# Optimization experiments

Hardware: AMD Instinct MI355X
Metric: run time of the kernel (lower is better)

Reference implementation:

```python
import jax, jax.numpy as jnp
import numpy as np

N_NODES = 100000
N_EDGES = 50000
NNZ = 1600000
IN_DIM, HID_DIM, N_CLASSES = 128, 128, 16


def setup_inputs() -> dict:
    key = jax.random.key(0)
    k1, k2, k3, k4, k5 = jax.random.split(key, 5)
    x = jax.random.normal(k1, (N_NODES, IN_DIM), dtype=jnp.float32)
    node_idx = jax.random.randint(k2, (NNZ,), 0, N_NODES, dtype=jnp.int64)
    edge_idx = jax.random.randint(k3, (NNZ,), 0, N_EDGES, dtype=jnp.int64)
    # glorot-ish weights, zero bias (PyG HypergraphConv: Linear(bias=False) + bias Parameter)
    W1 = jax.random.normal(k4, (IN_DIM, HID_DIM), dtype=jnp.float32) * (1.0 / np.sqrt(IN_DIM))
    b1 = jnp.zeros((HID_DIM,), dtype=jnp.float32)
    W2 = jax.random.normal(k5, (HID_DIM, N_CLASSES), dtype=jnp.float32) * (1.0 / np.sqrt(HID_DIM))
    b2 = jnp.zeros((N_CLASSES,), dtype=jnp.float32)
    return {"x": x, "node_idx": node_idx, "edge_idx": edge_idx, "num_edges": N_EDGES,
            "W1": W1, "b1": b1, "W2": W2, "b2": b2}


def hypergraph_conv(x, W, b, node_idx, edge_idx, num_edges):
    """PyG HypergraphConv (no attention, unit hyperedge weights):
       out = D^{-1} H B^{-1} H^T (x W) + b
    implemented as gather -> segment_sum (node->edge) -> gather -> segment_sum (edge->node)."""
    n_nodes = x.shape[0]
    ones = jnp.ones(node_idx.shape[0], dtype=x.dtype)
    deg = jax.ops.segment_sum(ones, node_idx, num_segments=n_nodes)      # D: node degree
    edeg = jax.ops.segment_sum(ones, edge_idx, num_segments=num_edges)   # B: hyperedge size
    Dinv = jnp.where(deg > 0, 1.0 / deg, 0.0)
    Binv = jnp.where(edeg > 0, 1.0 / edeg, 0.0)

    xw = x @ W                                                            # [N, F_out]
    # node -> hyperedge, norm = B^{-1} applied per message (indexed by edge)
    msg_ne = xw[node_idx] * Binv[edge_idx][:, None]                       # [nnz, F_out]
    e_feat = jax.ops.segment_sum(msg_ne, edge_idx, num_segments=num_edges)
    # hyperedge -> node, norm = D^{-1} applied per message (indexed by node)
    msg_en = e_feat[edge_idx] * Dinv[node_idx][:, None]                   # [nnz, F_out]
    out = jax.ops.segment_sum(msg_en, node_idx, num_segments=n_nodes)
    return out + b


def reference(x, node_idx, edge_idx, num_edges, W1, b1, W2, b2):
    # Dropout is inactive in eval mode; model is relu(conv1) -> conv2.
    h = jax.nn.relu(hypergraph_conv(x, W1, b1, node_idx, edge_idx, num_edges))
    return hypergraph_conv(h, W2, b2, node_idx, edge_idx, num_edges)
```

## Files before the change

### kernel.cpp

```cpp
#include <hip/hip_runtime.h>
#include <hip/hip_fp16.h>


#define N_EDGES_C 50000
#define F1 128
#define F2 16
#define CHUNK 4096
#define EBIN_SHIFT 7
#define NBIN_SHIFT 8
#define EBINS 391
#define NBINS 391

typedef __attribute__((ext_vector_type(8))) _Float16 half8;
typedef __attribute__((ext_vector_type(4))) float f32x4;
typedef unsigned short ushort16_t;


__global__ __launch_bounds__(256) void hist_chunk_kernel(
    const int* __restrict__ node_idx, const int* __restrict__ edge_idx,
    int* __restrict__ echunkcnt, int* __restrict__ nchunkcnt, int nnz) {
  __shared__ int ebc[EBINS], nbc[NBINS];
  const int t = threadIdx.x;
  for (int b = t; b < EBINS; b += 256) ebc[b] = 0;
  for (int b = t; b < NBINS; b += 256) nbc[b] = 0;
  __syncthreads();
  const int base = blockIdx.x * CHUNK;
  int end = base + CHUNK; if (end > nnz) end = nnz;
  for (int i = base + t; i < end; i += 256) {
    atomicAdd(&ebc[edge_idx[i] >> EBIN_SHIFT], 1);
    atomicAdd(&nbc[node_idx[i] >> NBIN_SHIFT], 1);
  }
  __syncthreads();
  const int nC = gridDim.x;
  for (int b = t; b < EBINS; b += 256) echunkcnt[b * nC + blockIdx.x] = ebc[b];
  for (int b = t; b < NBINS; b += 256) nchunkcnt[b * nC + blockIdx.x] = nbc[b];
}

__global__ __launch_bounds__(256) void cscan_p1_kernel(
    const int* __restrict__ ecc, const int* __restrict__ ncc,
    int* __restrict__ epart, int* __restrict__ npart,
    int Le, int Ln, int nbE) {
  __shared__ int red[256];
  const int t = threadIdx.x;
  const int b = blockIdx.x;
  const int* src; int L; int* dst; int bb;
  if (b < nbE) { src = ecc; L = Le; dst = epart; bb = b; }
  else         { src = ncc; L = Ln; dst = npart; bb = b - nbE; }
  int base = bb * 1024 + t * 4;
  int s = 0;
#pragma unroll
  for (int j = 0; j < 4; ++j) { int i = base + j; if (i < L) s += src[i]; }
  red[t] = s;
  __syncthreads();
  for (int d = 128; d > 0; d >>= 1) {
    if (t < d) red[t] += red[t + d];
    __syncthreads();
  }
  if (t == 0) dst[bb] = red[0];
}

__global__ __launch_bounds__(256) void cscan_p2_kernel(
    int* __restrict__ epart, int* __restrict__ npart,
    int* __restrict__ ebinbase, int* __restrict__ nbinbase,
    int nbE, int nbN, int nnz) {
  __shared__ int se[256], sn[256];
  const int t = threadIdx.x;
  se[t] = (t < nbE) ? epart[t] : 0;
  sn[t] = (t < nbN) ? npart[t] : 0;
  __syncthreads();
  for (int d = 1; d < 256; d <<= 1) {
    int ve = (t >= d) ? se[t - d] : 0;
    int vn = (t >= d) ? sn[t - d] : 0;
    __syncthreads();
    se[t] += ve; sn[t] += vn;
    __syncthreads();
  }
  if (t < nbE) epart[t] = (t > 0) ? se[t - 1] : 0;
  if (t < nbN) npart[t] = (t > 0) ? sn[t - 1] : 0;
  if (t == 0) { ebinbase[EBINS] = nnz; nbinbase[NBINS] = nnz; }
}

__global__ __launch_bounds__(256) void cscan_p3_kernel(
    const int* __restrict__ ecc, const int* __restrict__ ncc,
    const int* __restrict__ epart, const int* __restrict__ npart,
    int* __restrict__ erunoff, int* __restrict__ nrunoff,
    int* __restrict__ ebinbase, int* __restrict__ nbinbase,
    int Le, int Ln, int nbE, int nC) {
  __shared__ int red[256];
  const int t = threadIdx.x;
  const int b = blockIdx.x;
  const int* src; const int* part; int L; int* ro; int* bba; int bb;
  if (b < nbE) { src = ecc; part = epart; L = Le; ro = erunoff; bba = ebinbase; bb = b; }
  else         { src = ncc; part = npart; L = Ln; ro = nrunoff; bba = nbinbase; bb = b - nbE; }
  int base = bb * 1024 + t * 4;
  int v[4]; int s = 0;
#pragma unroll
  for (int j = 0; j < 4; ++j) { int i = base + j; v[j] = (i < L) ? src[i] : 0; s += v[j]; }
  red[t] = s;
  __syncthreads();
  for (int d = 1; d < 256; d <<= 1) {
    int x = (t >= d) ? red[t - d] : 0;
    __syncthreads();
    red[t] += x;
    __syncthreads();
  }
  int run = part[bb] + ((t > 0) ? red[t - 1] : 0);
#pragma unroll
  for (int j = 0; j < 4; ++j) {
    int i = base + j;
    if (i < L) {
      ro[i] = run;
      if (i % nC == 0) bba[i / nC] = run;
      run += v[j];
    }
  }
}


__global__ __launch_bounds__(256) void stage_kernel(
    const int* __restrict__ node_idx, const int* __restrict__ edge_idx,
    const int* __restrict__ erunoff, const int* __restrict__ nrunoff,
    unsigned* __restrict__ epairs, unsigned* __restrict__ npairs, int nnz) {
  __shared__ int ecur[EBINS], ncur[NBINS];
  const int t = threadIdx.x;
  const int nC = gridDim.x;
  for (int b = t; b < EBINS; b += 256) ecur[b] = erunoff[b * nC + blockIdx.x];
  for (int b = t; b < NBINS; b += 256) ncur[b] = nrunoff[b * nC + blockIdx.x];
  __syncthreads();
  const int base = blockIdx.x * CHUNK;
  int end = base + CHUNK; if (end > nnz) end = nnz;
  for (int i = base + t; i < end; i += 256) {
    int e = edge_idx[i];
    int n = node_idx[i];
    int p = atomicAdd(&ecur[e >> EBIN_SHIFT], 1);
    epairs[p] = ((unsigned)n << 7) | (unsigned)(e & 127);
    int q = atomicAdd(&ncur[n >> NBIN_SHIFT], 1);
    npairs[q] = ((unsigned)e << 8) | (unsigned)(n & 255);
  }
}

__global__ __launch_bounds__(256) void bin_scatter_kernel(
    const unsigned* __restrict__ epairs, const unsigned* __restrict__ npairs,
    const int* __restrict__ ebinbase, const int* __restrict__ nbinbase,
    int* __restrict__ eoff, int* __restrict__ noff,
    int* __restrict__ enbr, ushort16_t* __restrict__ nnbr,
    int n_edges, int n_nodes) {
  __shared__ int cnt[256];
  __shared__ int scn[256];
  const int bid = blockIdx.x;
  const int t = threadIdx.x;
  if (bid < EBINS) {
    const int e0 = bid << EBIN_SHIFT;
    const int ne = min(1 << EBIN_SHIFT, n_edges - e0);
    const int beg = ebinbase[bid], end = ebinbase[bid + 1];
    if (t < 128) cnt[t] = 0;
    __syncthreads();
    for (int j = beg + t; j < end; j += 256) atomicAdd(&cnt[epairs[j] & 127u], 1);
    __syncthreads();
    if (t < 128) scn[t] = cnt[t];
    __syncthreads();
    for (int d = 1; d < 128; d <<= 1) {
      int x = 0;
      if (t < 128 && t >= d) x = scn[t - d];
      __syncthreads();
      if (t < 128) scn[t] += x;
      __syncthreads();
    }
    int pos0 = 0;
    if (t < 128) {
      int excl = (t > 0) ? scn[t - 1] : 0;
      pos0 = beg + excl;
      if (t < ne) eoff[e0 + t] = pos0;
    }
    __syncthreads();
    if (t < 128) scn[t] = pos0;
    __syncthreads();
    for (int j = beg + t; j < end; j += 256) {
      unsigned p = epairs[j];
      int pos = atomicAdd(&scn[p & 127u], 1);
      enbr[pos] = (int)(p >> 7);
    }
    if (bid == EBINS - 1 && t == 0) eoff[n_edges] = end;
  } else {
    const int b = bid - EBINS;
    const int n0 = b << NBIN_SHIFT;
    const int nn = min(1 << NBIN_SHIFT, n_nodes - n0);
    const int beg = nbinbase[b], end = nbinbase[b + 1];
    cnt[t] = 0;
    __syncthreads();
    for (int j = beg + t; j < end; j += 256) atomicAdd(&cnt[npairs[j] & 255u], 1);
    __syncthreads();
    scn[t] = cnt[t];
    __syncthreads();
    for (int d = 1; d < 256; d <<= 1) {
      int x = (t >= d) ? scn[t - d] : 0;
      __syncthreads();
      scn[t] += x;
      __syncthreads();
    }
    int excl = (t > 0) ? scn[t - 1] : 0;
    int pos0 = beg + excl;
    if (t < nn) noff[n0 + t] = pos0;
    __syncthreads();
    scn[t] = pos0;
    __syncthreads();
    for (int j = beg + t; j < end; j += 256) {
      unsigned p = npairs[j];
      int pos = atomicAdd(&scn[p & 255u], 1);
      nnbr[pos] = (ushort16_t)(p >> 8);
    }
    if (bid == EBINS + NBINS - 1 && t == 0) noff[n_nodes] = end;
  }
}


__global__ __launch_bounds__(256) void w1t_kernel(
    const float* __restrict__ W1, __half* __restrict__ W1t) {
  int i = blockIdx.x * 256 + threadIdx.x;
  int n = i >> 7, k = i & 127;
  W1t[i] = __float2half(W1[k * 128 + n]);
}


__global__ __launch_bounds__(256) void gemm1_kernel(
    const float* __restrict__ A, const __half* __restrict__ W1t16,
    __half* __restrict__ C16, int M) {
  __shared__ _Float16 As[64 * 136];
  __shared__ _Float16 Bs[128 * 136];
  const int t = threadIdx.x;
  const int bm = blockIdx.x * 64;

#pragma unroll
  for (int i = 0; i < 8; ++i) {
    int lin = i * 256 + t;
    int row = lin >> 5;
    int c4 = lin & 31;
    int grow = bm + row;
    float4 v = make_float4(0.f, 0.f, 0.f, 0.f);
    if (grow < M) v = *(const float4*)(A + (size_t)grow * 128 + c4 * 4);
    _Float16* dst = &As[row * 136 + c4 * 4];
    dst[0] = (_Float16)v.x; dst[1] = (_Float16)v.y;
    dst[2] = (_Float16)v.z; dst[3] = (_Float16)v.w;
  }
#pragma unroll
  for (int i = 0; i < 8; ++i) {
    int lin = i * 256 + t;
    int n = lin >> 4;
    int c = lin & 15;
    *(float4*)&Bs[n * 136 + c * 8] = *(const float4*)(W1t16 + n * 128 + c * 8);
  }
  __syncthreads();

  const int w = t >> 6;
  const int lane = t & 63;
  const int l16 = lane & 15;
  const int quad = lane >> 4;

  f32x4 acc[8];
#pragma unroll
  for (int n = 0; n < 8; ++n) acc[n] = (f32x4){0.f, 0.f, 0.f, 0.f};

  const _Float16* arow = &As[(w * 16 + l16) * 136 + quad * 8];
#pragma unroll
  for (int kt = 0; kt < 4; ++kt) {
    half8 a = *(const half8*)(arow + kt * 32);
#pragma unroll
    for (int n = 0; n < 8; ++n) {
      half8 b = *(const half8*)&Bs[(n * 16 + l16) * 136 + kt * 32 + quad * 8];
      acc[n] = __builtin_amdgcn_mfma_f32_16x16x32_f16(a, b, acc[n], 0, 0, 0);
    }
  }
  __syncthreads();

#pragma unroll
  for (int n = 0; n < 8; ++n) {
#pragma unroll
    for (int r = 0; r < 4; ++r) {
      int row = w * 16 + quad * 4 + r;
      int col = n * 16 + l16;
      As[row * 136 + col] = (_Float16)acc[n][r];
    }
  }
  __syncthreads();

#pragma unroll
  for (int i = 0; i < 4; ++i) {
    int lin = i * 256 + t;
    int row = lin >> 4;
    int c = lin & 15;
    int grow = bm + row;
    if (grow < M)
      *(float4*)(C16 + (size_t)grow * 128 + c * 8) = *(const float4*)&As[row * 136 + c * 8];
  }
}


__device__ __forceinline__ void acc_mixw(float* ax, f32x4 v, float wt) {
  const unsigned* w = (const unsigned*)&v;
#pragma unroll
  for (int q = 0; q < 4; ++q) {
    asm("v_fma_mix_f32 %0, %1, %2, %0 op_sel:[0,0,0] op_sel_hi:[1,0,0]"
        : "+v"(ax[2 * q]) : "v"(w[q]), "v"(wt));
    asm("v_fma_mix_f32 %0, %1, %2, %0 op_sel:[1,0,0] op_sel_hi:[1,0,0]"
        : "+v"(ax[2 * q + 1]) : "v"(w[q]), "v"(wt));
  }
}

__device__ __forceinline__ void acc_mix1(float& alo, float& ahi, unsigned u, float wt) {
  asm("v_fma_mix_f32 %0, %1, %2, %0 op_sel:[0,0,0] op_sel_hi:[1,0,0]"
      : "+v"(alo) : "v"(u), "v"(wt));
  asm("v_fma_mix_f32 %0, %1, %2, %0 op_sel:[1,0,0] op_sel_hi:[1,0,0]"
      : "+v"(ahi) : "v"(u), "v"(wt));
}

__global__ __launch_bounds__(256) void edge_agg128_kernel(
    const f32x4* __restrict__ feat,
    const int* __restrict__ nbr, const int* __restrict__ off,
    float4* __restrict__ outf, int nseg) {
  int w = (blockIdx.x * 256 + threadIdx.x) >> 6;
  if (w >= nseg) return;
  const int lane = threadIdx.x & 63;
  const int r = lane >> 4;
  const int f = lane & 15;
  int beg = off[w], end = off[w + 1];
  const int kl = end - 1;
  float ax[8];
#pragma unroll
  for (int i = 0; i < 8; ++i) ax[i] = 0.f;
  for (int k = beg + r; k < end; k += 32) {
    int k1 = min(k + 4, kl),  k2 = min(k + 8, kl),  k3 = min(k + 12, kl);
    int k4 = min(k + 16, kl), k5 = min(k + 20, kl), k6 = min(k + 24, kl), k7 = min(k + 28, kl);
    float w1 = (k + 4 <= kl) ? 1.f : 0.f;
    float w2 = (k + 8 <= kl) ? 1.f : 0.f;
    float w3 = (k + 12 <= kl) ? 1.f : 0.f;
    float w4 = (k + 16 <= kl) ? 1.f : 0.f;
    float w5 = (k + 20 <= kl) ? 1.f : 0.f;
    float w6 = (k + 24 <= kl) ? 1.f : 0.f;
    float w7 = (k + 28 <= kl) ? 1.f : 0.f;
    int n0 = nbr[k],  n1 = nbr[k1], n2 = nbr[k2], n3 = nbr[k3];
    int n4 = nbr[k4], n5 = nbr[k5], n6 = nbr[k6], n7 = nbr[k7];
    f32x4 v0 = feat[(size_t)n0 * 16 + f];
    f32x4 v1 = feat[(size_t)n1 * 16 + f];
    f32x4 v2 = feat[(size_t)n2 * 16 + f];
    f32x4 v3 = feat[(size_t)n3 * 16 + f];
    f32x4 v4 = feat[(size_t)n4 * 16 + f];
    f32x4 v5 = feat[(size_t)n5 * 16 + f];
    f32x4 v6 = feat[(size_t)n6 * 16 + f];
    f32x4 v7 = feat[(size_t)n7 * 16 + f];
    asm volatile("" :: "v"(v0), "v"(v1), "v"(v2), "v"(v3),
                       "v"(v4), "v"(v5), "v"(v6), "v"(v7));
    acc_mixw(ax, v0, 1.f); acc_mixw(ax, v1, w1);
    acc_mixw(ax, v2, w2);  acc_mixw(ax, v3, w3);
    acc_mixw(ax, v4, w4);  acc_mixw(ax, v5, w5);
    acc_mixw(ax, v6, w6);  acc_mixw(ax, v7, w7);
  }
#pragma unroll
  for (int i = 0; i < 8; ++i) {
    ax[i] += __shfl_xor(ax[i], 16, 64);
    ax[i] += __shfl_xor(ax[i], 32, 64);
  }
  if (r == 0) {
    float inv = (end > beg) ? 1.f / (float)(end - beg) : 0.f;
    union { float4 f4; __half2 h[4]; } u;
#pragma unroll
    for (int q = 0; q < 4; ++q)
      u.h[q] = __floats2half2_rn(ax[2 * q] * inv, ax[2 * q + 1] * inv);
    outf[(size_t)w * 16 + f] = u.f4;
  }
}

__global__ __launch_bounds__(256) void node_agg128_kernel(
    const f32x4* __restrict__ feat,
    const ushort16_t* __restrict__ nbr, const int* __restrict__ off,
    const float* __restrict__ bias,
    float4* __restrict__ outf, int nseg) {
  int w = (blockIdx.x * 256 + threadIdx.x) >> 6;
  if (w >= nseg) return;
  const int lane = threadIdx.x & 63;
  const int r = lane >> 4;
  const int f = lane & 15;
  int beg = off[w], end = off[w + 1];
  const int kl = end - 1;
  float ax[8];
#pragma unroll
  for (int i = 0; i < 8; ++i) ax[i] = 0.f;
  for (int k = beg + r; k < end; k += 16) {
    int k1 = min(k + 4, kl), k2 = min(k + 8, kl), k3 = min(k + 12, kl);
    float w1 = (k + 4 <= kl) ? 1.f : 0.f;
    float w2 = (k + 8 <= kl) ? 1.f : 0.f;
    float w3 = (k + 12 <= kl) ? 1.f : 0.f;
    int e0 = nbr[k], e1 = nbr[k1], e2 = nbr[k2], e3 = nbr[k3];
    f32x4 v0 = feat[(size_t)e0 * 16 + f];
    f32x4 v1 = feat[(size_t)e1 * 16 + f];
    f32x4 v2 = feat[(size_t)e2 * 16 + f];
    f32x4 v3 = feat[(size_t)e3 * 16 + f];
    asm volatile("" :: "v"(v0), "v"(v1), "v"(v2), "v"(v3));
    acc_mixw(ax, v0, 1.f); acc_mixw(ax, v1, w1);
    acc_mixw(ax, v2, w2);  acc_mixw(ax, v3, w3);
  }
#pragma unroll
  for (int i = 0; i < 8; ++i) {
    ax[i] += __shfl_xor(ax[i], 16, 64);
    ax[i] += __shfl_xor(ax[i], 32, 64);
  }
  if (r == 0) {
    float inv = (end > beg) ? 1.f / (float)(end - beg) : 0.f;
    float4 blo = ((const float4*)bias)[2 * f];
    float4 bhi = ((const float4*)bias)[2 * f + 1];
    float bb[8] = {blo.x, blo.y, blo.z, blo.w, bhi.x, bhi.y, bhi.z, bhi.w};
    union { float4 f4; __half2 h[4]; } u;
#pragma unroll
    for (int q = 0; q < 4; ++q) {
      float hx = fmaxf(ax[2 * q] * inv + bb[2 * q], 0.f);
      float hy = fmaxf(ax[2 * q + 1] * inv + bb[2 * q + 1], 0.f);
      u.h[q] = __floats2half2_rn(hx, hy);
    }
    outf[(size_t)w * 16 + f] = u.f4;
  }
}


__global__ __launch_bounds__(256) void gemm2_kernel(
    const __half* __restrict__ H16, const float* __restrict__ W2,
    __half2* __restrict__ O16, int M) {
  __shared__ float ws2[128 * 16];
  const int t = threadIdx.x;
#pragma unroll
  for (int i = 0; i < 8; ++i) ws2[i * 256 + t] = W2[i * 256 + t];
  __syncthreads();

  int r0 = blockIdx.x * 512 + t;
  int r1 = r0 + 256;
  bool v0 = r0 < M, v1 = r1 < M;
  const __half2* h0 = (const __half2*)(H16 + (size_t)r0 * 128);
  const __half2* h1 = (const __half2*)(H16 + (size_t)r1 * 128);

  float4 acc0[4], acc1[4];
#pragma unroll
  for (int q = 0; q < 4; ++q) {
    acc0[q] = make_float4(0.f, 0.f, 0.f, 0.f);
    acc1[q] = make_float4(0.f, 0.f, 0.f, 0.f);
  }

  for (int k4 = 0; k4 < 32; ++k4) {
    float2 f00 = make_float2(0.f, 0.f), f01 = make_float2(0.f, 0.f);
    float2 f10 = make_float2(0.f, 0.f), f11 = make_float2(0.f, 0.f);
    if (v0) { f00 = __half22float2(h0[2 * k4]); f01 = __half22float2(h0[2 * k4 + 1]); }
    if (v1) { f10 = __half22float2(h1[2 * k4]); f11 = __half22float2(h1[2 * k4 + 1]); }
    const float a0s[4] = {f00.x, f00.y, f01.x, f01.y};
    const float a1s[4] = {f10.x, f10.y, f11.x, f11.y};
#pragma unroll
    for (int j = 0; j < 4; ++j) {
      int k = k4 * 4 + j;
#pragma unroll
      for (int q = 0; q < 4; ++q) {
        float4 b = *(const float4*)&ws2[k * 16 + q * 4];
        acc0[q].x = fmaf(a0s[j], b.x, acc0[q].x);
        acc0[q].y = fmaf(a0s[j], b.y, acc0[q].y);
        acc0[q].z = fmaf(a0s[j], b.z, acc0[q].z);
        acc0[q].w = fmaf(a0s[j], b.w, acc0[q].w);
        acc1[q].x = fmaf(a1s[j], b.x, acc1[q].x);
        acc1[q].y = fmaf(a1s[j], b.y, acc1[q].y);
        acc1[q].z = fmaf(a1s[j], b.z, acc1[q].z);
        acc1[q].w = fmaf(a1s[j], b.w, acc1[q].w);
      }
    }
  }
  if (v0) {
    __half2* op = O16 + (size_t)r0 * 8;
#pragma unroll
    for (int q = 0; q < 4; ++q) {
      op[q * 2]     = __floats2half2_rn(acc0[q].x, acc0[q].y);
      op[q * 2 + 1] = __floats2half2_rn(acc0[q].z, acc0[q].w);
    }
  }
  if (v1) {
    __half2* op = O16 + (size_t)r1 * 8;
#pragma unroll
    for (int q = 0; q < 4; ++q) {
      op[q * 2]     = __floats2half2_rn(acc1[q].x, acc1[q].y);
      op[q * 2 + 1] = __floats2half2_rn(acc1[q].z, acc1[q].w);
    }
  }
}


__global__ __launch_bounds__(256) void edge_agg16_kernel(
    const unsigned* __restrict__ feat,
    const int* __restrict__ nbr, const int* __restrict__ off,
    float* __restrict__ outf, int nseg) {
  int w = (blockIdx.x * 256 + threadIdx.x) >> 6;
  if (w >= nseg) return;
  const int lane = threadIdx.x & 63;
  const int r = lane >> 3;
  const int f = lane & 7;
  int beg = off[w], end = off[w + 1];
  const int kl = end - 1;
  float a0 = 0.f, a1 = 0.f;
  for (int k = beg + r; k < end; k += 32) {
    int k1 = min(k + 8, kl), k2 = min(k + 16, kl), k3 = min(k + 24, kl);
    float w1 = (k + 8 <= kl) ? 1.f : 0.f;
    float w2 = (k + 16 <= kl) ? 1.f : 0.f;
    float w3 = (k + 24 <= kl) ? 1.f : 0.f;
    int n0 = nbr[k], n1 = nbr[k1], n2 = nbr[k2], n3 = nbr[k3];
    unsigned u0 = feat[(size_t)n0 * 8 + f];
    unsigned u1 = feat[(size_t)n1 * 8 + f];
    unsigned u2 = feat[(size_t)n2 * 8 + f];
    unsigned u3 = feat[(size_t)n3 * 8 + f];
    asm volatile("" :: "v"(u0), "v"(u1), "v"(u2), "v"(u3));
    acc_mix1(a0, a1, u0, 1.f); acc_mix1(a0, a1, u1, w1);
    acc_mix1(a0, a1, u2, w2);  acc_mix1(a0, a1, u3, w3);
  }
  a0 += __shfl_xor(a0, 8, 64);  a1 += __shfl_xor(a1, 8, 64);
  a0 += __shfl_xor(a0, 16, 64); a1 += __shfl_xor(a1, 16, 64);
  a0 += __shfl_xor(a0, 32, 64); a1 += __shfl_xor(a1, 32, 64);
  if (r == 0) {
    float inv = (end > beg) ? 1.f / (float)(end - beg) : 0.f;
    ((float2*)outf)[(size_t)w * 8 + f] = make_float2(a0 * inv, a1 * inv);
  }
}

__global__ __launch_bounds__(256) void node_agg16_kernel(
    const float* __restrict__ feat,
    const ushort16_t* __restrict__ nbr, const int* __restrict__ off,
    const float* __restrict__ bias,
    float* __restrict__ outf, int nseg) {
  int w = (blockIdx.x * 256 + threadIdx.x) >> 6;
  if (w >= nseg) return;
  const int lane = threadIdx.x & 63;
  const int r = lane >> 4;
  const int f = lane & 15;
  int beg = off[w], end = off[w + 1];
  const int kl = end - 1;
  float a = 0.f;
  for (int k = beg + r; k < end; k += 16) {
    int k1 = min(k + 4, kl), k2 = min(k + 8, kl), k3 = min(k + 12, kl);
    float w1 = (k + 4 <= kl) ? 1.f : 0.f;
    float w2 = (k + 8 <= kl) ? 1.f : 0.f;
    float w3 = (k + 12 <= kl) ? 1.f : 0.f;
    int e0 = nbr[k], e1 = nbr[k1], e2 = nbr[k2], e3 = nbr[k3];
    float v0 = feat[(size_t)e0 * 16 + f];
    float v1 = feat[(size_t)e1 * 16 + f];
    float v2 = feat[(size_t)e2 * 16 + f];
    float v3 = feat[(size_t)e3 * 16 + f];
    asm volatile("" :: "v"(v0), "v"(v1), "v"(v2), "v"(v3));
    a += v0;
    a = fmaf(v1, w1, a);
    a = fmaf(v2, w2, a);
    a = fmaf(v3, w3, a);
  }
  a += __shfl_xor(a, 16, 64);
  a += __shfl_xor(a, 32, 64);
  if (r == 0) {
    float inv = (end > beg) ? 1.f / (float)(end - beg) : 0.f;
    outf[(size_t)w * 16 + f] = a * inv + bias[f];
  }
}


extern "C" void kernel_launch(void* const* d_in, const int* in_sizes, int n_in,
                              void* d_out, int out_size, void* d_ws, size_t ws_size,
                              hipStream_t stream) {
  const float* x        = (const float*)d_in[0];
  const int*   node_idx = (const int*)d_in[1];
  const int*   edge_idx = (const int*)d_in[2];
  const float* W1 = (const float*)d_in[4];
  const float* b1 = (const float*)d_in[5];
  const float* W2 = (const float*)d_in[6];
  const float* b2 = (const float*)d_in[7];
  float* out = (float*)d_out;

  const int n_nodes = in_sizes[0] / F1;
  const int nnz     = in_sizes[1];
  const int n_edges = N_EDGES_C;
  const int nC      = (nnz + CHUNK - 1) / CHUNK;
  const int Le      = EBINS * nC;
  const int Ln      = NBINS * nC;
  const int nbE     = (Le + 1023) / 1024;
  const int nbN     = (Ln + 1023) / 1024;

  char* ws = (char*)d_ws;
  unsigned* epairs = (unsigned*)(ws + 0);
  unsigned* npairs = (unsigned*)(ws + 6400000);
  __half*  h16    = (__half*)(ws + 0);
  __half*  xw16   = (__half*)(ws + 25600000);
  __half*  ef16   = (__half*)(ws + 51200000);
  __half*  hw216  = (__half*)(ws + 64000000);
  float*   ef2    = (float*)(ws + 70400000);
  int*     enbr   = (int*)(ws + 73600000);
  ushort16_t* nnbr16 = (ushort16_t*)(ws + 80000000);
  int*     eoff   = (int*)(ws + 86400000);
  int*     noff   = (int*)(ws + 86600008);
  int*     echunkcnt = (int*)(ws + 87000016);
  int*     nchunkcnt = (int*)(ws + 87611540);
  int*     erunoff   = (int*)(ws + 88223064);
  int*     nrunoff   = (int*)(ws + 88834588);
  int*     ebinbase  = (int*)(ws + 89446112);
  int*     nbinbase  = (int*)(ws + 89447680);
  int*     epart     = (int*)(ws + 89449248);
  int*     npart     = (int*)(ws + 89450272);
  __half*  w1t16     = (__half*)(ws + 89451520);

  w1t_kernel<<<64, 256, 0, stream>>>(W1, w1t16);

  hist_chunk_kernel<<<nC, 256, 0, stream>>>(node_idx, edge_idx,
                                            echunkcnt, nchunkcnt, nnz);
  cscan_p1_kernel<<<nbE + nbN, 256, 0, stream>>>(echunkcnt, nchunkcnt,
                                                 epart, npart, Le, Ln, nbE);
  cscan_p2_kernel<<<1, 256, 0, stream>>>(epart, npart, ebinbase, nbinbase,
                                         nbE, nbN, nnz);
  cscan_p3_kernel<<<nbE + nbN, 256, 0, stream>>>(echunkcnt, nchunkcnt,
                                                 epart, npart, erunoff, nrunoff,
                                                 ebinbase, nbinbase, Le, Ln, nbE, nC);
  stage_kernel<<<nC, 256, 0, stream>>>(node_idx, edge_idx, erunoff, nrunoff,
                                       epairs, npairs, nnz);
  bin_scatter_kernel<<<EBINS + NBINS, 256, 0, stream>>>(epairs, npairs,
                                                        ebinbase, nbinbase,
                                                        eoff, noff, enbr, nnbr16,
                                                        n_edges, n_nodes);

  gemm1_kernel<<<(n_nodes + 63) / 64, 256, 0, stream>>>(x, w1t16, xw16, n_nodes);
  edge_agg128_kernel<<<(n_edges * 64 + 255) / 256, 256, 0, stream>>>(
      (const f32x4*)xw16, enbr, eoff, (float4*)ef16, n_edges);
  node_agg128_kernel<<<(n_nodes * 64 + 255) / 256, 256, 0, stream>>>(
      (const f32x4*)ef16, nnbr16, noff, b1, (float4*)h16, n_nodes);

  gemm2_kernel<<<(n_nodes + 511) / 512, 256, 0, stream>>>(h16, W2,
                                                          (__half2*)hw216, n_nodes);
  edge_agg16_kernel<<<(n_edges * 64 + 255) / 256, 256, 0, stream>>>(
      (const unsigned*)hw216, enbr, eoff, ef2, n_edges);
  node_agg16_kernel<<<(n_nodes * 64 + 255) / 256, 256, 0, stream>>>(
      ef2, nnbr16, noff, b2, out, n_nodes);
}
```

Before: 367.1 us.

## Fuse second-layer GEMM into node aggregation and merge W1 transpose into histogram

The layer-1 node aggregation kernel now applies bias and ReLU, then multiplies the hidden row by W2 (staged in LDS in a permuted layout) with a shuffle reduction, writing the 16-wide fp16 result directly. This removes the fp16 hidden-state write and re-read plus the separate gemm2 launch. The W1 transpose is also folded into the histogram kernel as extra blocks, saving one launch. The price is extra LDS staging of W2 per block and shuffle work in the aggregation kernel.

```diff
diff --git a/kernel.cpp b/kernel.cpp
--- a/kernel.cpp
+++ b/kernel.cpp
@@ -16,9 +16,16 @@
 typedef unsigned short ushort16_t;
 
 
-__global__ __launch_bounds__(256) void hist_chunk_kernel(
+__global__ __launch_bounds__(256) void hist_w1t_kernel(
     const int* __restrict__ node_idx, const int* __restrict__ edge_idx,
-    int* __restrict__ echunkcnt, int* __restrict__ nchunkcnt, int nnz) {
+    int* __restrict__ echunkcnt, int* __restrict__ nchunkcnt, int nnz, int nC,
+    const float* __restrict__ W1, __half* __restrict__ W1t) {
+  if (blockIdx.x >= nC) {
+    int i = (blockIdx.x - nC) * 256 + threadIdx.x;
+    int n = i >> 7, k = i & 127;
+    W1t[i] = __float2half(W1[k * 128 + n]);
+    return;
+  }
   __shared__ int ebc[EBINS], nbc[NBINS];
   const int t = threadIdx.x;
   for (int b = t; b < EBINS; b += 256) ebc[b] = 0;
@@ -31,7 +38,6 @@
     atomicAdd(&nbc[node_idx[i] >> NBIN_SHIFT], 1);
   }
   __syncthreads();
-  const int nC = gridDim.x;
   for (int b = t; b < EBINS; b += 256) echunkcnt[b * nC + blockIdx.x] = ebc[b];
   for (int b = t; b < NBINS; b += 256) nchunkcnt[b * nC + blockIdx.x] = nbc[b];
 }
@@ -211,14 +217,6 @@
     }
     if (bid == EBINS + NBINS - 1 && t == 0) noff[n_nodes] = end;
   }
-}
-
-
-__global__ __launch_bounds__(256) void w1t_kernel(
-    const float* __restrict__ W1, __half* __restrict__ W1t) {
-  int i = blockIdx.x * 256 + threadIdx.x;
-  int n = i >> 7, k = i & 127;
-  W1t[i] = __float2half(W1[k * 128 + n]);
 }
 
 
@@ -369,11 +367,26 @@
   }
 }
 
-__global__ __launch_bounds__(256) void node_agg128_kernel(
+__global__ __launch_bounds__(256) void node_agg128_fused_kernel(
     const f32x4* __restrict__ feat,
     const ushort16_t* __restrict__ nbr, const int* __restrict__ off,
     const float* __restrict__ bias,
-    float4* __restrict__ outf, int nseg) {
+    const float* __restrict__ W2,
+    __half* __restrict__ out16,
+    int nseg) {
+  __shared__ float w2s[2048];
+  const int t = threadIdx.x;
+#pragma unroll
+  for (int i = 0; i < 8; ++i) {
+    int lin = i * 256 + t;
+    int plane = lin >> 6;
+    int slot  = lin & 63;
+    int j = plane >> 2, q = plane & 3;
+    int ff = slot >> 2, rr = slot & 3;
+    w2s[lin] = W2[(ff * 8 + j) * 16 + rr * 4 + q];
+  }
+  __syncthreads();
+
   int w = (blockIdx.x * 256 + threadIdx.x) >> 6;
   if (w >= nseg) return;
   const int lane = threadIdx.x & 63;
@@ -403,84 +416,33 @@
     ax[i] += __shfl_xor(ax[i], 16, 64);
     ax[i] += __shfl_xor(ax[i], 32, 64);
   }
-  if (r == 0) {
-    float inv = (end > beg) ? 1.f / (float)(end - beg) : 0.f;
-    float4 blo = ((const float4*)bias)[2 * f];
-    float4 bhi = ((const float4*)bias)[2 * f + 1];
-    float bb[8] = {blo.x, blo.y, blo.z, blo.w, bhi.x, bhi.y, bhi.z, bhi.w};
-    union { float4 f4; __half2 h[4]; } u;
-#pragma unroll
-    for (int q = 0; q < 4; ++q) {
-      float hx = fmaxf(ax[2 * q] * inv + bb[2 * q], 0.f);
-      float hy = fmaxf(ax[2 * q + 1] * inv + bb[2 * q + 1], 0.f);
-      u.h[q] = __floats2half2_rn(hx, hy);
-    }
-    outf[(size_t)w * 16 + f] = u.f4;
-  }
-}
-
-
-__global__ __launch_bounds__(256) void gemm2_kernel(
-    const __half* __restrict__ H16, const float* __restrict__ W2,
-    __half2* __restrict__ O16, int M) {
-  __shared__ float ws2[128 * 16];
-  const int t = threadIdx.x;
-#pragma unroll
-  for (int i = 0; i < 8; ++i) ws2[i * 256 + t] = W2[i * 256 + t];
-  __syncthreads();
-
-  int r0 = blockIdx.x * 512 + t;
-  int r1 = r0 + 256;
-  bool v0 = r0 < M, v1 = r1 < M;
-  const __half2* h0 = (const __half2*)(H16 + (size_t)r0 * 128);
-  const __half2* h1 = (const __half2*)(H16 + (size_t)r1 * 128);
-
-  float4 acc0[4], acc1[4];
-#pragma unroll
-  for (int q = 0; q < 4; ++q) {
-    acc0[q] = make_float4(0.f, 0.f, 0.f, 0.f);
-    acc1[q] = make_float4(0.f, 0.f, 0.f, 0.f);
-  }
-
-  for (int k4 = 0; k4 < 32; ++k4) {
-    float2 f00 = make_float2(0.f, 0.f), f01 = make_float2(0.f, 0.f);
-    float2 f10 = make_float2(0.f, 0.f), f11 = make_float2(0.f, 0.f);
-    if (v0) { f00 = __half22float2(h0[2 * k4]); f01 = __half22float2(h0[2 * k4 + 1]); }
-    if (v1) { f10 = __half22float2(h1[2 * k4]); f11 = __half22float2(h1[2 * k4 + 1]); }
-    const float a0s[4] = {f00.x, f00.y, f01.x, f01.y};
-    const float a1s[4] = {f10.x, f10.y, f11.x, f11.y};
-#pragma unroll
-    for (int j = 0; j < 4; ++j) {
-      int k = k4 * 4 + j;
-#pragma unroll
-      for (int q = 0; q < 4; ++q) {
-        float4 b = *(const float4*)&ws2[k * 16 + q * 4];
-        acc0[q].x = fmaf(a0s[j], b.x, acc0[q].x);
-        acc0[q].y = fmaf(a0s[j], b.y, acc0[q].y);
-        acc0[q].z = fmaf(a0s[j], b.z, acc0[q].z);
-        acc0[q].w = fmaf(a0s[j], b.w, acc0[q].w);
-        acc1[q].x = fmaf(a1s[j], b.x, acc1[q].x);
-        acc1[q].y = fmaf(a1s[j], b.y, acc1[q].y);
-        acc1[q].z = fmaf(a1s[j], b.z, acc1[q].z);
-        acc1[q].w = fmaf(a1s[j], b.w, acc1[q].w);
-      }
-    }
-  }
-  if (v0) {
-    __half2* op = O16 + (size_t)r0 * 8;
-#pragma unroll
-    for (int q = 0; q < 4; ++q) {
-      op[q * 2]     = __floats2half2_rn(acc0[q].x, acc0[q].y);
-      op[q * 2 + 1] = __floats2half2_rn(acc0[q].z, acc0[q].w);
-    }
-  }
-  if (v1) {
-    __half2* op = O16 + (size_t)r1 * 8;
-#pragma unroll
-    for (int q = 0; q < 4; ++q) {
-      op[q * 2]     = __floats2half2_rn(acc1[q].x, acc1[q].y);
-      op[q * 2 + 1] = __floats2half2_rn(acc1[q].z, acc1[q].w);
-    }
+  float inv = (end > beg) ? 1.f / (float)(end - beg) : 0.f;
+  float4 blo = ((const float4*)bias)[2 * f];
+  float4 bhi = ((const float4*)bias)[2 * f + 1];
+  float bb[8] = {blo.x, blo.y, blo.z, blo.w, bhi.x, bhi.y, bhi.z, bhi.w};
+  float h[8];
+#pragma unroll
+  for (int j = 0; j < 8; ++j) h[j] = fmaxf(ax[j] * inv + bb[j], 0.f);
+  float p0 = 0.f, p1 = 0.f, p2 = 0.f, p3 = 0.f;
+#pragma unroll
+  for (int j = 0; j < 8; ++j) {
+    const float* base = &w2s[j * 256 + f * 4 + r];
+    p0 = fmaf(h[j], base[0],   p0);
+    p1 = fmaf(h[j], base[64],  p1);
+    p2 = fmaf(h[j], base[128], p2);
+    p3 = fmaf(h[j], base[192], p3);
+  }
+#pragma unroll
+  for (int m = 1; m < 16; m <<= 1) {
+    p0 += __shfl_xor(p0, m, 64);
+    p1 += __shfl_xor(p1, m, 64);
+    p2 += __shfl_xor(p2, m, 64);
+    p3 += __shfl_xor(p3, m, 64);
+  }
+  if (f == 0) {
+    __half2* op = (__half2*)(out16 + (size_t)w * 16 + r * 4);
+    op[0] = __floats2half2_rn(p0, p1);
+    op[1] = __floats2half2_rn(p2, p3);
   }
 }
 
@@ -582,7 +544,6 @@
   char* ws = (char*)d_ws;
   unsigned* epairs = (unsigned*)(ws + 0);
   unsigned* npairs = (unsigned*)(ws + 6400000);
-  __half*  h16    = (__half*)(ws + 0);
   __half*  xw16   = (__half*)(ws + 25600000);
   __half*  ef16   = (__half*)(ws + 51200000);
   __half*  hw216  = (__half*)(ws + 64000000);
@@ -601,10 +562,9 @@
   int*     npart     = (int*)(ws + 89450272);
   __half*  w1t16     = (__half*)(ws + 89451520);
 
-  w1t_kernel<<<64, 256, 0, stream>>>(W1, w1t16);
-
-  hist_chunk_kernel<<<nC, 256, 0, stream>>>(node_idx, edge_idx,
-                                            echunkcnt, nchunkcnt, nnz);
+  hist_w1t_kernel<<<nC + 64, 256, 0, stream>>>(node_idx, edge_idx,
+                                               echunkcnt, nchunkcnt, nnz, nC,
+                                               W1, w1t16);
   cscan_p1_kernel<<<nbE + nbN, 256, 0, stream>>>(echunkcnt, nchunkcnt,
                                                  epart, npart, Le, Ln, nbE);
   cscan_p2_kernel<<<1, 256, 0, stream>>>(epart, npart, ebinbase, nbinbase,
@@ -622,11 +582,9 @@
   gemm1_kernel<<<(n_nodes + 63) / 64, 256, 0, stream>>>(x, w1t16, xw16, n_nodes);
   edge_agg128_kernel<<<(n_edges * 64 + 255) / 256, 256, 0, stream>>>(
       (const f32x4*)xw16, enbr, eoff, (float4*)ef16, n_edges);
-  node_agg128_kernel<<<(n_nodes * 64 + 255) / 256, 256, 0, stream>>>(
-      (const f32x4*)ef16, nnbr16, noff, b1, (float4*)h16, n_nodes);
-
-  gemm2_kernel<<<(n_nodes + 511) / 512, 256, 0, stream>>>(h16, W2,
-                                                          (__half2*)hw216, n_nodes);
+  node_agg128_fused_kernel<<<(n_nodes * 64 + 255) / 256, 256, 0, stream>>>(
+      (const f32x4*)ef16, nnbr16, noff, b1, W2, hw216, n_nodes);
+
   edge_agg16_kernel<<<(n_edges * 64 + 255) / 256, 256, 0, stream>>>(
       (const unsigned*)hw216, enbr, eoff, ef2, n_edges);
   node_agg16_kernel<<<(n_nodes * 64 + 255) / 256, 256, 0, stream>>>(
```

After: 409.7 us. 11.6% more time.

## Fuse W1 transpose into histogram and GEMM1 into staging kernel

Applied to the files above, without the earlier changes.

Merges the W1 transpose into the histogram launch as extra blocks, and merges the first GEMM into the stage kernel as extra blocks that share one dynamic shared-memory buffer. This removes two kernel launches and lets the independent GEMM run alongside the scatter-staging work. In exchange, the staging blocks now reserve GEMM-sized shared memory (about 52 KB), which can lower occupancy for the atomic-heavy staging path.

```diff
diff --git a/kernel.cpp b/kernel.cpp
--- a/kernel.cpp
+++ b/kernel.cpp
@@ -16,9 +16,16 @@
 typedef unsigned short ushort16_t;
 
 
-__global__ __launch_bounds__(256) void hist_chunk_kernel(
+__global__ __launch_bounds__(256) void hist_w1t_kernel(
     const int* __restrict__ node_idx, const int* __restrict__ edge_idx,
-    int* __restrict__ echunkcnt, int* __restrict__ nchunkcnt, int nnz) {
+    int* __restrict__ echunkcnt, int* __restrict__ nchunkcnt, int nnz, int nC,
+    const float* __restrict__ W1, __half* __restrict__ W1t) {
+  if (blockIdx.x >= nC) {
+    int i = (blockIdx.x - nC) * 256 + threadIdx.x;
+    int n = i >> 7, k = i & 127;
+    W1t[i] = __float2half(W1[k * 128 + n]);
+    return;
+  }
   __shared__ int ebc[EBINS], nbc[NBINS];
   const int t = threadIdx.x;
   for (int b = t; b < EBINS; b += 256) ebc[b] = 0;
@@ -31,7 +38,6 @@
     atomicAdd(&nbc[node_idx[i] >> NBIN_SHIFT], 1);
   }
   __syncthreads();
-  const int nC = gridDim.x;
   for (int b = t; b < EBINS; b += 256) echunkcnt[b * nC + blockIdx.x] = ebc[b];
   for (int b = t; b < NBINS; b += 256) nchunkcnt[b * nC + blockIdx.x] = nbc[b];
 }
@@ -117,25 +123,100 @@
 }
 
 
-__global__ __launch_bounds__(256) void stage_kernel(
+__global__ __launch_bounds__(256) void stage_gemm1_kernel(
     const int* __restrict__ node_idx, const int* __restrict__ edge_idx,
     const int* __restrict__ erunoff, const int* __restrict__ nrunoff,
-    unsigned* __restrict__ epairs, unsigned* __restrict__ npairs, int nnz) {
-  __shared__ int ecur[EBINS], ncur[NBINS];
+    unsigned* __restrict__ epairs, unsigned* __restrict__ npairs,
+    int nnz, int nC,
+    const float* __restrict__ A, const __half* __restrict__ W1t16,
+    __half* __restrict__ C16, int M) {
+  __shared__ __align__(16) char smem[52224];
   const int t = threadIdx.x;
-  const int nC = gridDim.x;
-  for (int b = t; b < EBINS; b += 256) ecur[b] = erunoff[b * nC + blockIdx.x];
-  for (int b = t; b < NBINS; b += 256) ncur[b] = nrunoff[b * nC + blockIdx.x];
-  __syncthreads();
-  const int base = blockIdx.x * CHUNK;
-  int end = base + CHUNK; if (end > nnz) end = nnz;
-  for (int i = base + t; i < end; i += 256) {
-    int e = edge_idx[i];
-    int n = node_idx[i];
-    int p = atomicAdd(&ecur[e >> EBIN_SHIFT], 1);
-    epairs[p] = ((unsigned)n << 7) | (unsigned)(e & 127);
-    int q = atomicAdd(&ncur[n >> NBIN_SHIFT], 1);
-    npairs[q] = ((unsigned)e << 8) | (unsigned)(n & 255);
+
+  if (blockIdx.x < nC) {
+    int* ecur = (int*)smem;
+    int* ncur = (int*)(smem + EBINS * 4);
+    for (int b = t; b < EBINS; b += 256) ecur[b] = erunoff[b * nC + blockIdx.x];
+    for (int b = t; b < NBINS; b += 256) ncur[b] = nrunoff[b * nC + blockIdx.x];
+    __syncthreads();
+    const int base = blockIdx.x * CHUNK;
+    int end = base + CHUNK; if (end > nnz) end = nnz;
+    for (int i = base + t; i < end; i += 256) {
+      int e = edge_idx[i];
+      int n = node_idx[i];
+      int p = atomicAdd(&ecur[e >> EBIN_SHIFT], 1);
+      epairs[p] = ((unsigned)n << 7) | (unsigned)(e & 127);
+      int q = atomicAdd(&ncur[n >> NBIN_SHIFT], 1);
+      npairs[q] = ((unsigned)e << 8) | (unsigned)(n & 255);
+    }
+    return;
+  }
+
+  _Float16* As = (_Float16*)smem;
+  _Float16* Bs = (_Float16*)(smem + 17408);
+  const int bm = (blockIdx.x - nC) * 64;
+
+#pragma unroll
+  for (int i = 0; i < 8; ++i) {
+    int lin = i * 256 + t;
+    int row = lin >> 5;
+    int c4 = lin & 31;
+    int grow = bm + row;
+    float4 v = make_float4(0.f, 0.f, 0.f, 0.f);
+    if (grow < M) v = *(const float4*)(A + (size_t)grow * 128 + c4 * 4);
+    _Float16* dst = &As[row * 136 + c4 * 4];
+    dst[0] = (_Float16)v.x; dst[1] = (_Float16)v.y;
+    dst[2] = (_Float16)v.z; dst[3] = (_Float16)v.w;
+  }
+#pragma unroll
+  for (int i = 0; i < 8; ++i) {
+    int lin = i * 256 + t;
+    int n = lin >> 4;
+    int c = lin & 15;
+    *(float4*)&Bs[n * 136 + c * 8] = *(const float4*)(W1t16 + n * 128 + c * 8);
+  }
+  __syncthreads();
+
+  const int w = t >> 6;
+  const int lane = t & 63;
+  const int l16 = lane & 15;
+  const int quad = lane >> 4;
+
+  f32x4 acc[8];
+#pragma unroll
+  for (int n = 0; n < 8; ++n) acc[n] = (f32x4){0.f, 0.f, 0.f, 0.f};
+
+  const _Float16* arow = &As[(w * 16 + l16) * 136 + quad * 8];
+#pragma unroll
+  for (int kt = 0; kt < 4; ++kt) {
+    half8 a = *(const half8*)(arow + kt * 32);
+#pragma unroll
+    for (int n = 0; n < 8; ++n) {
+      half8 b = *(const half8*)&Bs[(n * 16 + l16) * 136 + kt * 32 + quad * 8];
+      acc[n] = __builtin_amdgcn_mfma_f32_16x16x32_f16(a, b, acc[n], 0, 0, 0);
+    }
+  }
+  __syncthreads();
+
+#pragma unroll
+  for (int n = 0; n < 8; ++n) {
+#pragma unroll
+    for (int r = 0; r < 4; ++r) {
+      int row = w * 16 + quad * 4 + r;
+      int col = n * 16 + l16;
+      As[row * 136 + col] = (_Float16)acc[n][r];
+    }
+  }
+  __syncthreads();
+
+#pragma unroll
+  for (int i = 0; i < 4; ++i) {
+    int lin = i * 256 + t;
+    int row = lin >> 4;
+    int c = lin & 15;
+    int grow = bm + row;
+    if (grow < M)
+      *(float4*)(C16 + (size_t)grow * 128 + c * 8) = *(const float4*)&As[row * 136 + c * 8];
   }
 }
 
@@ -210,87 +291,6 @@
       nnbr[pos] = (ushort16_t)(p >> 8);
     }
     if (bid == EBINS + NBINS - 1 && t == 0) noff[n_nodes] = end;
-  }
-}
-
-
-__global__ __launch_bounds__(256) void w1t_kernel(
-    const float* __restrict__ W1, __half* __restrict__ W1t) {
-  int i = blockIdx.x * 256 + threadIdx.x;
-  int n = i >> 7, k = i & 127;
-  W1t[i] = __float2half(W1[k * 128 + n]);
-}
-
-
-__global__ __launch_bounds__(256) void gemm1_kernel(
-    const float* __restrict__ A, const __half* __restrict__ W1t16,
-    __half* __restrict__ C16, int M) {
-  __shared__ _Float16 As[64 * 136];
-  __shared__ _Float16 Bs[128 * 136];
-  const int t = threadIdx.x;
-  const int bm = blockIdx.x * 64;
-
-#pragma unroll
-  for (int i = 0; i < 8; ++i) {
-    int lin = i * 256 + t;
-    int row = lin >> 5;
-    int c4 = lin & 31;
-    int grow = bm + row;
-    float4 v = make_float4(0.f, 0.f, 0.f, 0.f);
-    if (grow < M) v = *(const float4*)(A + (size_t)grow * 128 + c4 * 4);
-    _Float16* dst = &As[row * 136 + c4 * 4];
-    dst[0] = (_Float16)v.x; dst[1] = (_Float16)v.y;
-    dst[2] = (_Float16)v.z; dst[3] = (_Float16)v.w;
-  }
-#pragma unroll
-  for (int i = 0; i < 8; ++i) {
-    int lin = i * 256 + t;
-    int n = lin >> 4;
-    int c = lin & 15;
-    *(float4*)&Bs[n * 136 + c * 8] = *(const float4*)(W1t16 + n * 128 + c * 8);
-  }
-  __syncthreads();
-
-  const int w = t >> 6;
-  const int lane = t & 63;
-  const int l16 = lane & 15;
-  const int quad = lane >> 4;
-
-  f32x4 acc[8];
-#pragma unroll
-  for (int n = 0; n < 8; ++n) acc[n] = (f32x4){0.f, 0.f, 0.f, 0.f};
-
-  const _Float16* arow = &As[(w * 16 + l16) * 136 + quad * 8];
-#pragma unroll
-  for (int kt = 0; kt < 4; ++kt) {
-    half8 a = *(const half8*)(arow + kt * 32);
-#pragma unroll
-    for (int n = 0; n < 8; ++n) {
-      half8 b = *(const half8*)&Bs[(n * 16 + l16) * 136 + kt * 32 + quad * 8];
-      acc[n] = __builtin_amdgcn_mfma_f32_16x16x32_f16(a, b, acc[n], 0, 0, 0);
-    }
-  }
-  __syncthreads();
-
-#pragma unroll
-  for (int n = 0; n < 8; ++n) {
-#pragma unroll
-    for (int r = 0; r < 4; ++r) {
-      int row = w * 16 + quad * 4 + r;
-      int col = n * 16 + l16;
-      As[row * 136 + col] = (_Float16)acc[n][r];
-    }
-  }
-  __syncthreads();
-
-#pragma unroll
-  for (int i = 0; i < 4; ++i) {
-    int lin = i * 256 + t;
-    int row = lin >> 4;
-    int c = lin & 15;
-    int grow = bm + row;
-    if (grow < M)
-      *(float4*)(C16 + (size_t)grow * 128 + c * 8) = *(const float4*)&As[row * 136 + c * 8];
   }
 }
 
@@ -601,10 +601,9 @@
   int*     npart     = (int*)(ws + 89450272);
   __half*  w1t16     = (__half*)(ws + 89451520);
 
-  w1t_kernel<<<64, 256, 0, stream>>>(W1, w1t16);
-
-  hist_chunk_kernel<<<nC, 256, 0, stream>>>(node_idx, edge_idx,
-                                            echunkcnt, nchunkcnt, nnz);
+  hist_w1t_kernel<<<nC + 64, 256, 0, stream>>>(node_idx, edge_idx,
+                                               echunkcnt, nchunkcnt, nnz, nC,
+                                               W1, w1t16);
   cscan_p1_kernel<<<nbE + nbN, 256, 0, stream>>>(echunkcnt, nchunkcnt,
                                                  epart, npart, Le, Ln, nbE);
   cscan_p2_kernel<<<1, 256, 0, stream>>>(epart, npart, ebinbase, nbinbase,
@@ -612,14 +611,14 @@
   cscan_p3_kernel<<<nbE + nbN, 256, 0, stream>>>(echunkcnt, nchunkcnt,
                                                  epart, npart, erunoff, nrunoff,
                                                  ebinbase, nbinbase, Le, Ln, nbE, nC);
-  stage_kernel<<<nC, 256, 0, stream>>>(node_idx, edge_idx, erunoff, nrunoff,
-                                       epairs, npairs, nnz);
+  stage_gemm1_kernel<<<nC + (n_nodes + 63) / 64, 256, 0, stream>>>(
+      node_idx, edge_idx, erunoff, nrunoff, epairs, npairs, nnz, nC,
+      x, w1t16, xw16, n_nodes);
   bin_scatter_kernel<<<EBINS + NBINS, 256, 0, stream>>>(epairs, npairs,
                                                         ebinbase, nbinbase,
                                                         eoff, noff, enbr, nnbr16,
                                                         n_edges, n_nodes);
 
-  gemm1_kernel<<<(n_nodes + 63) / 64, 256, 0, stream>>>(x, w1t16, xw16, n_nodes);
   edge_agg128_kernel<<<(n_edges * 64 + 255) / 256, 256, 0, stream>>>(
       (const f32x4*)xw16, enbr, eoff, (float4*)ef16, n_edges);
   node_agg128_kernel<<<(n_nodes * 64 + 255) / 256, 256, 0, stream>>>(
```

Result: no change. 363.9 us (-0.9%).
